# Performance work log

Measured on AMD Instinct MI355X. Metric: run time of the kernel, lower is better.

Reference implementation:

```python
import jax, jax.numpy as jnp
import numpy as np

DIM = 4096
NH = 32
NKV = 8
HD = DIM // NH          # 128
REP = NH // NKV          # 4
B = 1
T = 2048
THETA = 500000.0
NEG = -1e9


def setup_inputs() -> dict:
    key = jax.random.key(0)
    ks = jax.random.split(key, 6)
    x = jax.random.normal(ks[0], (B, T, DIM), jnp.float32)
    # RoPE tables (real/imag parts of freqs_cis = exp(i * t * inv_freq))
    inv_freq = 1.0 / (THETA ** (np.arange(0, HD, 2, dtype=np.float32) / HD))  # (HD/2,)
    ang = np.outer(np.arange(T, dtype=np.float32), inv_freq)                  # (T, HD/2)
    freqs_cos = jnp.asarray(np.cos(ang), jnp.float32)
    freqs_sin = jnp.asarray(np.sin(ang), jnp.float32)
    # additive causal mask for prefill (pos=0): (T, T)
    mask = jnp.where(np.tril(np.ones((T, T), dtype=bool)), 0.0, NEG).astype(jnp.float32)
    cache_k = jnp.zeros((B, T, NKV, HD), jnp.float32)
    cache_v = jnp.zeros((B, T, NKV, HD), jnp.float32)
    s = 0.02
    wk_w = jax.random.normal(ks[1], (NKV * HD, DIM), jnp.float32) * s
    wk_b = jnp.zeros((NKV * HD,), jnp.float32)
    wv_w = jax.random.normal(ks[2], (NKV * HD, DIM), jnp.float32) * s
    wv_b = jnp.zeros((NKV * HD,), jnp.float32)
    wo_w = jax.random.normal(ks[3], (DIM, DIM), jnp.float32) * s
    wo_b = jnp.zeros((DIM,), jnp.float32)
    return dict(x=x, freqs_cos=freqs_cos, freqs_sin=freqs_sin, mask=mask,
                cache_k=cache_k, cache_v=cache_v,
                wk_w=wk_w, wk_b=wk_b, wv_w=wv_w, wv_b=wv_b,
                wo_w=wo_w, wo_b=wo_b, pos=0)


def _rope(t, cos, sin):
    # t: (B, T, H, HD); pairs (even, odd) form complex numbers
    tr = t.reshape(*t.shape[:-1], HD // 2, 2)
    re, im = tr[..., 0], tr[..., 1]
    c = cos[None, :, None, :]
    s = sin[None, :, None, :]
    out = jnp.stack([re * c - im * s, re * s + im * c], axis=-1)
    return out.reshape(t.shape)


def reference(x, freqs_cos, freqs_sin, mask, cache_k, cache_v,
              wk_w, wk_b, wv_w, wv_b, wo_w, wo_b, pos):
    Bx, Tx, D = x.shape
    # NOTE: faithful to source bug -- q projection uses wo (shared with output proj)
    q = x @ wo_w.T + wo_b                        # (B, T, D)
    k = x @ wk_w.T + wk_b                        # (B, T, NKV*HD)
    v = x @ wv_w.T + wv_b
    q = q.reshape(Bx, Tx, NH, HD)
    k = k.reshape(Bx, Tx, NKV, HD)
    v = v.reshape(Bx, Tx, NKV, HD)
    q = _rope(q, freqs_cos, freqs_sin)
    k = _rope(k, freqs_cos, freqs_sin)
    # KV-cache append then read back [:pos+T]
    ck = cache_k.at[:Bx, pos:pos + Tx].set(k)
    cv = cache_v.at[:Bx, pos:pos + Tx].set(v)
    k = ck[:Bx, :pos + Tx]
    v = cv[:Bx, :pos + Tx]
    # repeat_kv (GQA expansion)
    k = jnp.repeat(k, REP, axis=2)               # (B, S, NH, HD)
    v = jnp.repeat(v, REP, axis=2)
    scale = 1.0 / jnp.sqrt(jnp.float32(HD))
    scores = jnp.einsum('bqhd,bkhd->bhqk', q, k) * scale
    scores = scores + mask[None, None, :, :]
    p = jax.nn.softmax(scores.astype(jnp.float32), axis=-1)
    out = jnp.einsum('bhqk,bkhd->bqhd', p, v).reshape(Bx, Tx, D)
    return out @ wo_w.T + wo_b
```

## Files before the change

### kernel.cpp

```cpp
#include <hip/hip_runtime.h>
#include <stdint.h>
#include <stddef.h>

#define T_SEQ 2048
#define DIM   4096
#define NH    32
#define NKV   8
#define HD    128
#define KVD   (NKV*HD)

typedef __attribute__((ext_vector_type(8))) short short8;
typedef __attribute__((ext_vector_type(4))) float floatx4;

static __device__ __forceinline__ float bf2f(short u) {
    union { unsigned int i; float f; } c; c.i = ((unsigned int)(unsigned short)u) << 16; return c.f;
}
static __device__ __forceinline__ short f2bf(float f) {
    union { float f; unsigned int u; } c; c.f = f;
    unsigned int r = c.u + 0x7fff + ((c.u >> 16) & 1);
    return (short)(r >> 16);
}
static __device__ __forceinline__ short8 ld8_f2b(const float* p) {
    floatx4 a = *(const floatx4*)p;
    floatx4 b = *(const floatx4*)(p + 4);
    short8 r;
    r[0]=f2bf(a[0]); r[1]=f2bf(a[1]); r[2]=f2bf(a[2]); r[3]=f2bf(a[3]);
    r[4]=f2bf(b[0]); r[5]=f2bf(b[1]); r[6]=f2bf(b[2]); r[7]=f2bf(b[3]);
    return r;
}

#define GLD16(g, l) __builtin_amdgcn_global_load_lds( \
    (const __attribute__((address_space(1))) unsigned int*)(g), \
    (__attribute__((address_space(3))) unsigned int*)(l), 16, 0, 0)

template<int CTRL>
static __device__ __forceinline__ float dppf(float x) {
    return __int_as_float(__builtin_amdgcn_update_dpp(
        0, __float_as_int(x), CTRL, 0xf, 0xf, true));
}
static __device__ __forceinline__ float rowmax16(float x) {
    x = fmaxf(x, dppf<0xB1>(x));
    x = fmaxf(x, dppf<0x4E>(x));
    x = fmaxf(x, dppf<0x141>(x));
    x = fmaxf(x, dppf<0x140>(x));
    return x;
}
static __device__ __forceinline__ float rowsum16(float x) {
    x += dppf<0xB1>(x);
    x += dppf<0x4E>(x);
    x += dppf<0x141>(x);
    x += dppf<0x140>(x);
    return x;
}

__global__ __launch_bounds__(256)
void cvt_bf16(const float* __restrict__ x, const float* __restrict__ wk,
              const float* __restrict__ wv, const float* __restrict__ wo,
              short* __restrict__ xb, short* __restrict__ wkb,
              short* __restrict__ wvb, short* __restrict__ wob) {
    size_t i8 = ((size_t)blockIdx.x * 256 + threadIdx.x) * 8;
    const float* src; short* dst; size_t off;
    if (i8 < 8388608)        { src = x;  dst = xb;  off = i8; }
    else if (i8 < 12582912)  { src = wk; dst = wkb; off = i8 - 8388608; }
    else if (i8 < 16777216)  { src = wv; dst = wvb; off = i8 - 12582912; }
    else                     { src = wo; dst = wob; off = i8 - 16777216; }
    *(short8*)(dst + off) = ld8_f2b(src + off);
}

template<bool C_F32>
static __device__ __forceinline__
void gemm_core(const short* __restrict__ A, const short* __restrict__ B,
               const float* __restrict__ bias, void* __restrict__ Cp,
               int N, int K, int bm, int bn) {
    __shared__ short sA[128*32];
    __shared__ short sB[128*32];
    const int tid  = threadIdx.x;
    const int wave = tid >> 6, lane = tid & 63;
    const int l15  = lane & 15, lq = lane >> 4;
    const int wm   = (wave >> 1) * 64, wn = (wave & 1) * 64;

    floatx4 acc[4][4];
    #pragma unroll
    for (int i = 0; i < 4; i++)
        #pragma unroll
        for (int j = 0; j < 4; j++)
            acc[i][j] = (floatx4)(0.0f);

    const int c0 = tid, c1 = 256 + tid;
    const int r0 = c0 >> 2, k0 = (c0 & 3) * 8;
    const int r1 = c1 >> 2, k1 = (c1 & 3) * 8;
    const short* pA0 = A + (size_t)(bm + r0) * K + k0;
    const short* pA1 = A + (size_t)(bm + r1) * K + k1;
    const short* pB0 = B + (size_t)(bn + r0) * K + k0;
    const short* pB1 = B + (size_t)(bn + r1) * K + k1;

    for (int kt = 0; kt < K; kt += 32) {
        __syncthreads();
        GLD16(pA0 + kt, &sA[c0 * 8]);
        GLD16(pA1 + kt, &sA[c1 * 8]);
        GLD16(pB0 + kt, &sB[c0 * 8]);
        GLD16(pB1 + kt, &sB[c1 * 8]);
        __syncthreads();

        short8 af[4], bfr[4];
        #pragma unroll
        for (int mi = 0; mi < 4; mi++)
            af[mi] = *(const short8*)&sA[(wm + mi*16 + l15)*32 + lq*8];
        #pragma unroll
        for (int ni = 0; ni < 4; ni++)
            bfr[ni] = *(const short8*)&sB[(wn + ni*16 + l15)*32 + lq*8];
        #pragma unroll
        for (int mi = 0; mi < 4; mi++)
            #pragma unroll
            for (int ni = 0; ni < 4; ni++)
                acc[mi][ni] = __builtin_amdgcn_mfma_f32_16x16x32_bf16(af[mi], bfr[ni], acc[mi][ni], 0, 0, 0);
    }

    #pragma unroll
    for (int ni = 0; ni < 4; ni++) {
        int col = bn + wn + ni*16 + l15;
        float bv = bias[col];
        #pragma unroll
        for (int mi = 0; mi < 4; mi++) {
            int row = bm + wm + mi*16 + lq*4;
            #pragma unroll
            for (int r = 0; r < 4; r++) {
                float v = acc[mi][ni][r] + bv;
                if (C_F32) ((float*)Cp)[(size_t)(row + r)*N + col] = v;
                else       ((short*)Cp)[(size_t)(row + r)*N + col] = f2bf(v);
            }
        }
    }
}

template<bool C_F32>
__global__ __launch_bounds__(256)
void gemm_bt(const short* __restrict__ A, const short* __restrict__ B,
             const float* __restrict__ bias, void* __restrict__ Cp,
             int N, int K) {
    gemm_core<C_F32>(A, B, bias, Cp, N, K, blockIdx.y * 128, blockIdx.x * 128);
}

__global__ __launch_bounds__(256)
void gemm_kv(const short* __restrict__ A,
             const short* __restrict__ Bk, const float* __restrict__ bk, short* __restrict__ Ck,
             const short* __restrict__ Bv, const float* __restrict__ bv, short* __restrict__ Cv) {
    const short* B = blockIdx.z ? Bv : Bk;
    const float* bias = blockIdx.z ? bv : bk;
    short* C = blockIdx.z ? Cv : Ck;
    gemm_core<false>(A, B, bias, C, KVD, DIM, blockIdx.y * 128, blockIdx.x * 128);
}

__global__ __launch_bounds__(256)
void rope_k(short* __restrict__ Q, short* __restrict__ Kc,
            const float* __restrict__ fc, const float* __restrict__ fs) {
    int idx = blockIdx.x * 256 + threadIdx.x;
    const int NQ = T_SEQ * NH  * (HD/2);
    const int NK = T_SEQ * NKV * (HD/2);
    short* base; int t, i; size_t off;
    if (idx < NQ) {
        i = idx & 63;
        int th = idx >> 6;
        t = th >> 5;
        off = (size_t)th * HD + i*2;
        base = Q;
    } else if (idx < NQ + NK) {
        int kidx = idx - NQ;
        i = kidx & 63;
        int th = kidx >> 6;
        t = th >> 3;
        off = (size_t)th * HD + i*2;
        base = Kc;
    } else return;
    float re = bf2f(base[off]), im = bf2f(base[off+1]);
    float c = fc[t*64 + i], s = fs[t*64 + i];
    base[off]   = f2bf(re*c - im*s);
    base[off+1] = f2bf(re*s + im*c);
}

__global__ __launch_bounds__(256)
void vtrans(const short* __restrict__ V, short* __restrict__ Vt) {
    __shared__ short sT[64*72];
    const int tid = threadIdx.x;
    const int bt = blockIdx.x, bd = blockIdx.y;
    #pragma unroll
    for (int i = 0; i < 2; i++) {
        int c = i*256 + tid;
        int r = c >> 3, c8 = (c & 7) * 8;
        *(short8*)&sT[r*72 + c8] = *(const short8*)(V + (size_t)(bt*64 + r)*KVD + bd*64 + c8);
    }
    __syncthreads();
    #pragma unroll
    for (int i = 0; i < 2; i++) {
        int c = i*256 + tid;
        int d = c >> 3, t8 = (c & 7) * 8;
        short8 o;
        #pragma unroll
        for (int j = 0; j < 8; j++) o[j] = sT[(t8 + j)*72 + d];
        *(short8*)(Vt + (size_t)(bd*64 + d)*T_SEQ + bt*64 + t8) = o;
    }
}

#define ROWK 136
#define ROWV 72

__global__ __launch_bounds__(256, 2)
void flash_attn(const short* __restrict__ Q, const short* __restrict__ Kc,
                const short* __restrict__ Vt, short* __restrict__ O) {
    __shared__ short sK[64*ROWK];
    __shared__ short sV[128*ROWV];
    __shared__ short sP[4*2048];
    const int tid  = threadIdx.x;
    const int wave = tid >> 6, lane = tid & 63;
    const int l15  = lane & 15, lq = lane >> 4;
    const int kvg  = blockIdx.y;
    const int qt   = (blockIdx.y < 4) ? (int)blockIdx.x : 63 - (int)blockIdx.x;
    const int hl   = wave;
    const int qb   = qt * 32;
    const float scale = 0.08838834764831845f;

    short8 qf[2][4];
    #pragma unroll
    for (int mi = 0; mi < 2; mi++)
        #pragma unroll
        for (int ks = 0; ks < 4; ks++)
            qf[mi][ks] = *(const short8*)(Q + (size_t)(qb + mi*16 + l15)*DIM
                                          + kvg*512 + hl*128 + ks*32 + lq*8);

    short* sPw = sP + wave*2048;

    float m_r[2][4], l_r[2][4];
    floatx4 o_acc[2][8];
    #pragma unroll
    for (int mi = 0; mi < 2; mi++) {
        #pragma unroll
        for (int r = 0; r < 4; r++) { m_r[mi][r] = -1e30f; l_r[mi][r] = 0.0f; }
        #pragma unroll
        for (int nd = 0; nd < 8; nd++) o_acc[mi][nd] = (floatx4)(0.0f);
    }

    const int ktmax = qt >> 1;
    for (int kt = 0; kt <= ktmax; kt++) {
        short8 kbuf[4], vbuf[4];
        #pragma unroll
        for (int i = 0; i < 4; i++) {
            int c = i*256 + tid;
            int r = c >> 4, c8 = (c & 15) * 8;
            kbuf[i] = *(const short8*)(Kc + (size_t)(kt*64 + r)*KVD + kvg*HD + c8);
            int rv = c >> 3, v8 = (c & 7) * 8;
            vbuf[i] = *(const short8*)(Vt + (size_t)(kvg*HD + rv)*T_SEQ + kt*64 + v8);
        }
        __syncthreads();
        #pragma unroll
        for (int i = 0; i < 4; i++) {
            int c = i*256 + tid;
            int r = c >> 4, c8 = (c & 15) * 8;
            *(short8*)&sK[r*ROWK + c8] = kbuf[i];
            int rv = c >> 3, v8 = (c & 7) * 8;
            *(short8*)&sV[rv*ROWV + v8] = vbuf[i];
        }
        __syncthreads();

        floatx4 s_acc[2][4];
        #pragma unroll
        for (int mi = 0; mi < 2; mi++)
            #pragma unroll
            for (int ni = 0; ni < 4; ni++) s_acc[mi][ni] = (floatx4)(0.0f);
        __builtin_amdgcn_s_setprio(1);
        #pragma unroll
        for (int ks = 0; ks < 4; ks++)
            #pragma unroll
            for (int ni = 0; ni < 4; ni++) {
                short8 kf = *(const short8*)&sK[(ni*16 + l15)*ROWK + ks*32 + lq*8];
                s_acc[0][ni] = __builtin_amdgcn_mfma_f32_16x16x32_bf16(qf[0][ks], kf, s_acc[0][ni], 0, 0, 0);
                s_acc[1][ni] = __builtin_amdgcn_mfma_f32_16x16x32_bf16(qf[1][ks], kf, s_acc[1][ni], 0, 0, 0);
            }
        __builtin_amdgcn_s_setprio(0);

        const bool last = (kt == ktmax);

        #pragma unroll
        for (int mi = 0; mi < 2; mi++) {
            float sv[4][4], mx[4];
            #pragma unroll
            for (int r = 0; r < 4; r++) mx[r] = -1e30f;
            #pragma unroll
            for (int ni = 0; ni < 4; ni++) {
                int col = kt*64 + ni*16 + l15;
                #pragma unroll
                for (int r = 0; r < 4; r++) {
                    float x = s_acc[mi][ni][r] * scale;
                    if (last) {
                        int row = qb + mi*16 + lq*4 + r;
                        x = (col <= row) ? x : -1e30f;
                    }
                    sv[ni][r] = x;
                    mx[r] = fmaxf(mx[r], x);
                }
            }
            #pragma unroll
            for (int r = 0; r < 4; r++) mx[r] = rowmax16(mx[r]);

            float g = fmaxf(fmaxf(mx[0] - m_r[mi][0], mx[1] - m_r[mi][1]),
                            fmaxf(mx[2] - m_r[mi][2], mx[3] - m_r[mi][3]));
            if (__any(g > 8.0f)) {
                #pragma unroll
                for (int r = 0; r < 4; r++) {
                    float mn = fmaxf(m_r[mi][r], mx[r]);
                    float a  = __expf(m_r[mi][r] - mn);
                    m_r[mi][r] = mn;
                    l_r[mi][r] *= a;
                    #pragma unroll
                    for (int nd = 0; nd < 8; nd++) o_acc[mi][nd][r] *= a;
                }
            }

            float rs[4] = {0.0f, 0.0f, 0.0f, 0.0f};
            #pragma unroll
            for (int ni = 0; ni < 4; ni++)
                #pragma unroll
                for (int r = 0; r < 4; r++) {
                    float p = __expf(sv[ni][r] - m_r[mi][r]);
                    sv[ni][r] = p;
                    rs[r] += p;
                }
            #pragma unroll
            for (int r = 0; r < 4; r++) {
                rs[r] = rowsum16(rs[r]);
                l_r[mi][r] += rs[r];
            }

            #pragma unroll
            for (int ni = 0; ni < 4; ni++)
                #pragma unroll
                for (int r = 0; r < 4; r++) {
                    int q = mi*16 + lq*4 + r, k = ni*16 + l15;
                    sPw[q*64 + (((k >> 3) ^ (q & 7))*8) + (k & 7)] = f2bf(sv[ni][r]);
                }
        }

        __builtin_amdgcn_s_setprio(1);
        #pragma unroll
        for (int ks = 0; ks < 2; ks++) {
            int kk = ks*32 + lq*8;
            short8 pf[2];
            #pragma unroll
            for (int mi = 0; mi < 2; mi++) {
                int q = mi*16 + l15;
                pf[mi] = *(const short8*)&sPw[q*64 + (((kk >> 3) ^ (q & 7))*8)];
            }
            #pragma unroll
            for (int nd = 0; nd < 8; nd++) {
                short8 vf = *(const short8*)&sV[(nd*16 + l15)*ROWV + kk];
                o_acc[0][nd] = __builtin_amdgcn_mfma_f32_16x16x32_bf16(pf[0], vf, o_acc[0][nd], 0, 0, 0);
                o_acc[1][nd] = __builtin_amdgcn_mfma_f32_16x16x32_bf16(pf[1], vf, o_acc[1][nd], 0, 0, 0);
            }
        }
        __builtin_amdgcn_s_setprio(0);
    }

    #pragma unroll
    for (int mi = 0; mi < 2; mi++)
        #pragma unroll
        for (int nd = 0; nd < 8; nd++) {
            int col = (kvg*4 + hl)*HD + nd*16 + l15;
            #pragma unroll
            for (int r = 0; r < 4; r++) {
                int row = qb + mi*16 + lq*4 + r;
                O[(size_t)row*DIM + col] = f2bf(o_acc[mi][nd][r] / l_r[mi][r]);
            }
        }
}

extern "C" void kernel_launch(void* const* d_in, const int* in_sizes, int n_in,
                              void* d_out, int out_size, void* d_ws, size_t ws_size,
                              hipStream_t stream) {
    const float* x    = (const float*)d_in[0];
    const float* fc   = (const float*)d_in[1];
    const float* fs   = (const float*)d_in[2];
    const float* wk_w = (const float*)d_in[6];
    const float* wk_b = (const float*)d_in[7];
    const float* wv_w = (const float*)d_in[8];
    const float* wv_b = (const float*)d_in[9];
    const float* wo_w = (const float*)d_in[10];
    const float* wo_b = (const float*)d_in[11];
    float* out = (float*)d_out;

    short* xb  = (short*)d_ws;
    short* wkb = xb  + 8388608;
    short* wvb = wkb + 4194304;
    short* wob = wvb + 4194304;
    short* Q   = wob + 16777216;
    short* K   = Q   + 8388608;
    short* V   = K   + 2097152;
    short* Vt  = V   + 2097152;
    short* AO  = Vt  + 2097152;

    cvt_bf16<<<dim3(16384), dim3(256), 0, stream>>>(x, wk_w, wv_w, wo_w, xb, wkb, wvb, wob);

    gemm_bt<false><<<dim3(32, 16), dim3(256), 0, stream>>>(xb, wob, wo_b, Q, DIM, DIM);
    gemm_kv<<<dim3(8, 16, 2), dim3(256), 0, stream>>>(xb, wkb, wk_b, K, wvb, wv_b, V);

    int nrope = T_SEQ*NH*(HD/2) + T_SEQ*NKV*(HD/2);
    rope_k<<<dim3((nrope + 255)/256), dim3(256), 0, stream>>>(Q, K, fc, fs);

    vtrans<<<dim3(32, 16), dim3(256), 0, stream>>>(V, Vt);

    flash_attn<<<dim3(64, 8), dim3(256), 0, stream>>>(Q, K, Vt, AO);

    gemm_bt<true><<<dim3(32, 16), dim3(256), 0, stream>>>(AO, wob, wo_b, out, DIM, DIM);
}
```

Measured before the change: 567.0 us.

## Merge Q/K/V projections into one launch and split-K the output GEMM

Q, K and V projections now run in one 48x16 grid instead of two launches, which fills the device better and removes a launch. The output projection is split along K into two halves (1024 blocks instead of 512) that accumulate into the output with atomicAdd. The output is first seeded with the bias by a separate kernel. This adds an extra write pass over the output, fp32 atomic traffic, and a result whose summation order is not deterministic.

```diff
diff --git a/kernel.cpp b/kernel.cpp
--- a/kernel.cpp
+++ b/kernel.cpp
@@ -67,11 +67,20 @@
     *(short8*)(dst + off) = ld8_f2b(src + off);
 }
 
-template<bool C_F32>
+__global__ __launch_bounds__(256)
+void bias_init(const float* __restrict__ b, float* __restrict__ out) {
+    size_t i = (size_t)blockIdx.x * 256 + threadIdx.x;
+    int col4 = (int)((i * 4) & (DIM - 1));
+    floatx4 v;
+    v[0] = b[col4]; v[1] = b[col4+1]; v[2] = b[col4+2]; v[3] = b[col4+3];
+    *(floatx4*)(out + i * 4) = v;
+}
+
+template<int CMODE>
 static __device__ __forceinline__
 void gemm_core(const short* __restrict__ A, const short* __restrict__ B,
                const float* __restrict__ bias, void* __restrict__ Cp,
-               int N, int K, int bm, int bn) {
+               int N, int K, int LD, int bm, int bn) {
     __shared__ short sA[128*32];
     __shared__ short sB[128*32];
     const int tid  = threadIdx.x;
@@ -89,10 +98,10 @@
     const int c0 = tid, c1 = 256 + tid;
     const int r0 = c0 >> 2, k0 = (c0 & 3) * 8;
     const int r1 = c1 >> 2, k1 = (c1 & 3) * 8;
-    const short* pA0 = A + (size_t)(bm + r0) * K + k0;
-    const short* pA1 = A + (size_t)(bm + r1) * K + k1;
-    const short* pB0 = B + (size_t)(bn + r0) * K + k0;
-    const short* pB1 = B + (size_t)(bn + r1) * K + k1;
+    const short* pA0 = A + (size_t)(bm + r0) * LD + k0;
+    const short* pA1 = A + (size_t)(bm + r1) * LD + k1;
+    const short* pB0 = B + (size_t)(bn + r0) * LD + k0;
+    const short* pB1 = B + (size_t)(bn + r1) * LD + k1;
 
     for (int kt = 0; kt < K; kt += 32) {
         __syncthreads();
@@ -119,36 +128,40 @@
     #pragma unroll
     for (int ni = 0; ni < 4; ni++) {
         int col = bn + wn + ni*16 + l15;
-        float bv = bias[col];
+        float bv = (CMODE == 2) ? 0.0f : bias[col];
         #pragma unroll
         for (int mi = 0; mi < 4; mi++) {
             int row = bm + wm + mi*16 + lq*4;
             #pragma unroll
             for (int r = 0; r < 4; r++) {
                 float v = acc[mi][ni][r] + bv;
-                if (C_F32) ((float*)Cp)[(size_t)(row + r)*N + col] = v;
-                else       ((short*)Cp)[(size_t)(row + r)*N + col] = f2bf(v);
-            }
-        }
-    }
-}
-
-template<bool C_F32>
-__global__ __launch_bounds__(256)
-void gemm_bt(const short* __restrict__ A, const short* __restrict__ B,
-             const float* __restrict__ bias, void* __restrict__ Cp,
-             int N, int K) {
-    gemm_core<C_F32>(A, B, bias, Cp, N, K, blockIdx.y * 128, blockIdx.x * 128);
-}
-
-__global__ __launch_bounds__(256)
-void gemm_kv(const short* __restrict__ A,
-             const short* __restrict__ Bk, const float* __restrict__ bk, short* __restrict__ Ck,
-             const short* __restrict__ Bv, const float* __restrict__ bv, short* __restrict__ Cv) {
-    const short* B = blockIdx.z ? Bv : Bk;
-    const float* bias = blockIdx.z ? bv : bk;
-    short* C = blockIdx.z ? Cv : Ck;
-    gemm_core<false>(A, B, bias, C, KVD, DIM, blockIdx.y * 128, blockIdx.x * 128);
+                if (CMODE == 1)      ((float*)Cp)[(size_t)(row + r)*N + col] = v;
+                else if (CMODE == 0) ((short*)Cp)[(size_t)(row + r)*N + col] = f2bf(v);
+                else atomicAdd(&((float*)Cp)[(size_t)(row + r)*N + col], v);
+            }
+        }
+    }
+}
+
+__global__ __launch_bounds__(256)
+void gemm_qkv(const short* __restrict__ A,
+              const short* __restrict__ Bq, const float* __restrict__ bq, short* __restrict__ Cq,
+              const short* __restrict__ Bk, const float* __restrict__ bk, short* __restrict__ Ck,
+              const short* __restrict__ Bv, const float* __restrict__ bv, short* __restrict__ Cv) {
+    const int ct = blockIdx.x;
+    const short* B; const float* bias; short* C; int N, bn;
+    if (ct < 32)      { B = Bq; bias = bq; C = Cq; N = DIM; bn = ct*128; }
+    else if (ct < 40) { B = Bk; bias = bk; C = Ck; N = KVD; bn = (ct-32)*128; }
+    else              { B = Bv; bias = bv; C = Cv; N = KVD; bn = (ct-40)*128; }
+    gemm_core<0>(A, B, bias, C, N, DIM, DIM, blockIdx.y * 128, bn);
+}
+
+__global__ __launch_bounds__(256)
+void gemm_out_sk(const short* __restrict__ A, const short* __restrict__ B,
+                 float* __restrict__ Cp) {
+    const int kh = blockIdx.z;
+    gemm_core<2>(A + kh*(DIM/2), B + kh*(DIM/2), nullptr, Cp,
+                 DIM, DIM/2, DIM, blockIdx.y * 128, blockIdx.x * 128);
 }
 
 __global__ __launch_bounds__(256)
@@ -398,8 +411,10 @@
 
     cvt_bf16<<<dim3(16384), dim3(256), 0, stream>>>(x, wk_w, wv_w, wo_w, xb, wkb, wvb, wob);
 
-    gemm_bt<false><<<dim3(32, 16), dim3(256), 0, stream>>>(xb, wob, wo_b, Q, DIM, DIM);
-    gemm_kv<<<dim3(8, 16, 2), dim3(256), 0, stream>>>(xb, wkb, wk_b, K, wvb, wv_b, V);
+    bias_init<<<dim3(T_SEQ*DIM/4/256), dim3(256), 0, stream>>>(wo_b, out);
+
+    gemm_qkv<<<dim3(48, 16), dim3(256), 0, stream>>>(
+        xb, wob, wo_b, Q, wkb, wk_b, K, wvb, wv_b, V);
 
     int nrope = T_SEQ*NH*(HD/2) + T_SEQ*NKV*(HD/2);
     rope_k<<<dim3((nrope + 255)/256), dim3(256), 0, stream>>>(Q, K, fc, fs);
@@ -408,5 +423,5 @@
 
     flash_attn<<<dim3(64, 8), dim3(256), 0, stream>>>(Q, K, Vt, AO);
 
-    gemm_bt<true><<<dim3(32, 16), dim3(256), 0, stream>>>(AO, wob, wo_b, out, DIM, DIM);
-}
+    gemm_out_sk<<<dim3(32, 16, 2), dim3(256), 0, stream>>>(AO, wob, out);
+}
```

New measurement: 595.8 us. +5.1%, slower.

## Double-buffer LDS tiles in GEMM core to overlap loads with MFMA

Applied to the files above, without the earlier changes.

Splits the shared-memory A/B tiles into two buffers and issues the global-to-LDS loads for the next K-slice before computing on the current one. This hides global load latency behind the MFMA work and needs one barrier per slice instead of two. It doubles LDS use per block, which may lower occupancy. It also relies on the direct-to-LDS loads being complete by the barrier and assumes the K-slice count is even.

```diff
diff --git a/kernel.cpp b/kernel.cpp
--- a/kernel.cpp
+++ b/kernel.cpp
@@ -72,8 +72,10 @@
 void gemm_core(const short* __restrict__ A, const short* __restrict__ B,
                const float* __restrict__ bias, void* __restrict__ Cp,
                int N, int K, int bm, int bn) {
-    __shared__ short sA[128*32];
-    __shared__ short sB[128*32];
+    __shared__ short sA0[128*32];
+    __shared__ short sA1[128*32];
+    __shared__ short sB0[128*32];
+    __shared__ short sB1[128*32];
     const int tid  = threadIdx.x;
     const int wave = tid >> 6, lane = tid & 63;
     const int l15  = lane & 15, lq = lane >> 4;
@@ -94,26 +96,38 @@
     const short* pB0 = B + (size_t)(bn + r0) * K + k0;
     const short* pB1 = B + (size_t)(bn + r1) * K + k1;
 
-    for (int kt = 0; kt < K; kt += 32) {
-        __syncthreads();
-        GLD16(pA0 + kt, &sA[c0 * 8]);
-        GLD16(pA1 + kt, &sA[c1 * 8]);
-        GLD16(pB0 + kt, &sB[c0 * 8]);
-        GLD16(pB1 + kt, &sB[c1 * 8]);
-        __syncthreads();
-
+    auto stage = [&](short* dA, short* dB, int kt) {
+        GLD16(pA0 + kt, dA + c0 * 8);
+        GLD16(pA1 + kt, dA + c1 * 8);
+        GLD16(pB0 + kt, dB + c0 * 8);
+        GLD16(pB1 + kt, dB + c1 * 8);
+    };
+    auto compute = [&](const short* dA, const short* dB) {
         short8 af[4], bfr[4];
         #pragma unroll
         for (int mi = 0; mi < 4; mi++)
-            af[mi] = *(const short8*)&sA[(wm + mi*16 + l15)*32 + lq*8];
+            af[mi] = *(const short8*)&dA[(wm + mi*16 + l15)*32 + lq*8];
         #pragma unroll
         for (int ni = 0; ni < 4; ni++)
-            bfr[ni] = *(const short8*)&sB[(wn + ni*16 + l15)*32 + lq*8];
+            bfr[ni] = *(const short8*)&dB[(wn + ni*16 + l15)*32 + lq*8];
         #pragma unroll
         for (int mi = 0; mi < 4; mi++)
             #pragma unroll
             for (int ni = 0; ni < 4; ni++)
                 acc[mi][ni] = __builtin_amdgcn_mfma_f32_16x16x32_bf16(af[mi], bfr[ni], acc[mi][ni], 0, 0, 0);
+    };
+
+    stage(sA0, sB0, 0);
+    __syncthreads();
+
+    const int nt = K >> 5;
+    for (int t = 0; t < nt; t += 2) {
+        stage(sA1, sB1, (t + 1) * 32);
+        compute(sA0, sB0);
+        __syncthreads();
+        if (t + 2 < nt) stage(sA0, sB0, (t + 2) * 32);
+        compute(sA1, sB1);
+        __syncthreads();
     }
 
     #pragma unroll
```

Result: faster. 530.3 us (-6.5%).
